# Kernel optimization log

Hardware: AMD Instinct MI355X
Metric: run time of the kernel (lower is better)

## Reference

```python
import jax, jax.numpy as jnp
import numpy as np

EPS = 1e-12  # F.normalize default eps


def setup_inputs() -> dict:
    key = jax.random.key(0)
    x = jax.random.normal(key, (10000, 512), dtype=jnp.float32)
    return {"x": x, "k": 9}


def reference(x, k):
    # F.normalize(x, p=2, dim=0): L2-normalize each feature column over points
    col_norm = jnp.sqrt(jnp.sum(x * x, axis=0, keepdims=True))  # [1, D]
    xn = x / jnp.maximum(col_norm, EPS)                          # [N, D]

    # pairwise squared euclidean distance: ||xi||^2 - 2 xi.xj + ||xj||^2
    sq = jnp.sum(xn * xn, axis=-1, keepdims=True)                # [N, 1]
    dist = sq - 2.0 * (xn @ xn.T) + sq.T                          # [N, N]

    # k nearest neighbors = top-k of negative distance
    _, nn_idx = jax.lax.top_k(-dist, k)                           # [N, k] int32

    n = x.shape[0]
    center_idx = jnp.broadcast_to(jnp.arange(n, dtype=nn_idx.dtype)[:, None], (n, k))
    edge_idx = jnp.stack((nn_idx, center_idx), axis=0)            # [2, N, k]
    return edge_idx
```

## Files before the change

### kernel.cpp

```cpp
#include <hip/hip_runtime.h>
#include <math.h>

#define DD 512
#define NBLKA 400

#define PM 128
#define PN 128
#define KB 32
#define CSPLIT 6
#define NC 12
#define PBUF 32
#define PBSTRIDE 36
#define NCTOT (CSPLIT*NC)
#define KOUTMAX 16
#define RS_MARGIN 2e-4f

typedef __attribute__((ext_vector_type(8))) short bf16x8;
typedef __attribute__((ext_vector_type(4))) float f32x4;

static __device__ __forceinline__ unsigned short f2bf(float f) {
    unsigned u = __float_as_uint(f);
    u += 0x7fff + ((u >> 16) & 1);
    return (unsigned short)(u >> 16);
}

__global__ void colsum_partial(const float* __restrict__ x, double* __restrict__ partial,
                               int N, int rows_per_block) {
    int b = blockIdx.x;
    int t = threadIdx.x;
    int r0 = b * rows_per_block;
    int r1 = min(r0 + rows_per_block, N);
    double s0 = 0.0, s1 = 0.0;
    for (int r = r0; r < r1; ++r) {
        float v0 = x[(size_t)r * DD + t];
        float v1 = x[(size_t)r * DD + t + 256];
        s0 += (double)v0 * (double)v0;
        s1 += (double)v1 * (double)v1;
    }
    partial[(size_t)b * DD + t]       = s0;
    partial[(size_t)b * DD + t + 256] = s1;
}

__global__ void colnorm_finish(const double* __restrict__ partial, double* __restrict__ rn,
                               double* __restrict__ w, int nblk) {
    int c = threadIdx.x;
    double s = 0.0;
    for (int b = 0; b < nblk; ++b) s += partial[(size_t)b * DD + c];
    double n = fmax(sqrt(s), 1e-12);
    double r = 1.0 / n;
    rn[c]  = r;
    w[c]   = r * r;
}

__global__ __launch_bounds__(256) void row_sq(const float* __restrict__ x,
                       const double* __restrict__ rn,
                       double* __restrict__ sq, float* __restrict__ sqf,
                       unsigned short* __restrict__ xnbf, int N) {
    int lane = threadIdx.x & 63;
    int wid  = threadIdx.x >> 6;
    int i = blockIdx.x * 4 + wid;
    if (i >= N) return;

    const float4* xr = (const float4*)(x + (size_t)i * DD);
    float4 v0 = xr[lane];
    float4 v1 = xr[64 + lane];
    const double2* rp = (const double2*)rn;
    double2 r0a = rp[lane * 2],       r0b = rp[lane * 2 + 1];
    double2 r1a = rp[128 + lane * 2], r1b = rp[128 + lane * 2 + 1];

    double a0 = (double)v0.x * r0a.x, a1 = (double)v0.y * r0a.y;
    double a2 = (double)v0.z * r0b.x, a3 = (double)v0.w * r0b.y;
    double b0 = (double)v1.x * r1a.x, b1 = (double)v1.y * r1a.y;
    double b2 = (double)v1.z * r1b.x, b3 = (double)v1.w * r1b.y;

    ushort4 s0 = { f2bf((float)a0), f2bf((float)a1), f2bf((float)a2), f2bf((float)a3) };
    ushort4 s1 = { f2bf((float)b0), f2bf((float)b1), f2bf((float)b2), f2bf((float)b3) };
    *(ushort4*)(xnbf + (size_t)i * DD + lane * 4)       = s0;
    *(ushort4*)(xnbf + (size_t)i * DD + 256 + lane * 4) = s1;

    double loc = a0*a0 + a1*a1 + a2*a2 + a3*a3 + b0*b0 + b1*b1 + b2*b2 + b3*b3;
#pragma unroll
    for (int off = 32; off > 0; off >>= 1)
        loc += __shfl_xor(loc, off, 64);
    if (lane == 0) { sq[i] = loc; sqf[i] = (float)loc; }
}

__global__ __launch_bounds__(256, 2) void gemm_prefilter(
    const unsigned short* __restrict__ xnbf,
    const float* __restrict__ sqf, int* __restrict__ cand, float* __restrict__ cands,
    int N, int ntileM, int ntileN)
{
    __shared__ __align__(16) unsigned char lds_raw[65536];
    __shared__ float sqi_s[PM];
    __shared__ float sqj_s[PN];
    __shared__ float thr_s[PM];
    __shared__ int   cnt_s[PM];
    __shared__ int   flag_s;

    float (*Bsc)[PBSTRIDE] = (float (*)[PBSTRIDE]) lds_raw;
    int   (*Bid)[PBSTRIDE] = (int   (*)[PBSTRIDE]) (lds_raw + 32768);

    const int bid   = blockIdx.x;
    const int q     = bid & 7;
    const int s     = bid >> 3;
    const int ridx  = s / CSPLIT;
    const int split = s - ridx * CSPLIT;
    const int rowb  = q + 8 * ridx;
    if (rowb >= ntileM) return;
    const int row0  = rowb * PM;

    const int t      = threadIdx.x;
    const int lane15 = t & 15;
    const int quad   = (t >> 4) & 3;
    const int wave   = t >> 6;
    const int wr     = (wave >> 1) * 64;
    const int wc     = (wave & 1) * 64;
    const int sl     = quad ^ (lane15 & 3);

    if (t == 0) flag_s = 0;
    if (t < PM) {
        int i = row0 + t;
        sqi_s[t] = (i < N) ? sqf[i] : 0.f;
        thr_s[t] = __builtin_inff();
        cnt_s[t] = 0;
    }

    float ls[NC];
    int   li[NC];
#pragma unroll
    for (int m = 0; m < NC; ++m) { ls[m] = __builtin_inff(); li[m] = 0x7fffffff; }

    f32x4 acc[4][4];

    for (int tile = split; tile < ntileN; tile += CSPLIT) {
        int col0 = tile * PN;

        if (t < PN) {
            int j = col0 + t;
            sqj_s[t] = (j < N) ? sqf[j] : __builtin_inff();
        }
        __syncthreads();

#pragma unroll
        for (int mt = 0; mt < 4; ++mt)
#pragma unroll
            for (int nt = 0; nt < 4; ++nt)
                acc[mt][nt] = (f32x4){0.f, 0.f, 0.f, 0.f};

        auto STAGE = [&](int kc, int buf) {
#pragma unroll
            for (int l = 0; l < 4; ++l) {
                int e      = t + l * 256;
                int region = e >> 9;
                int re     = e & 511;
                int row    = re >> 2;
                int c      = (re & 3) ^ (row & 3);
                int basei  = region ? col0 : row0;
                size_t g = (size_t)(basei + row) * DD + kc + c * 8;
                __builtin_amdgcn_global_load_lds(
                    (const unsigned int*)(xnbf + g),
                    (unsigned int*)(lds_raw + (size_t)buf * 16384 + (size_t)e * 16), 16, 0, 0);
            }
        };

        STAGE(0, 0); STAGE(KB, 1); STAGE(2 * KB, 2);
#pragma unroll 1
        for (int cc = 0; cc < 16; ++cc) {
            if (cc <= 13)      asm volatile("s_waitcnt vmcnt(8)" ::: "memory");
            else if (cc == 14) asm volatile("s_waitcnt vmcnt(4)" ::: "memory");
            else               asm volatile("s_waitcnt vmcnt(0)" ::: "memory");
            __builtin_amdgcn_s_barrier();
            __builtin_amdgcn_sched_barrier(0);
            if (cc + 3 < 16)
                STAGE((cc + 3) * KB, (cc + 3) & 3);
            __builtin_amdgcn_sched_barrier(0);

            const unsigned char* rb = lds_raw + (size_t)(cc & 3) * 16384;
            bf16x8 af[4], bfg[4];
#pragma unroll
            for (int mt = 0; mt < 4; ++mt)
                af[mt] = *(const bf16x8*)(rb + (size_t)(wr + mt * 16 + lane15) * 64 + sl * 16);
#pragma unroll
            for (int nt = 0; nt < 4; ++nt)
                bfg[nt] = *(const bf16x8*)(rb + 8192 + (size_t)(wc + nt * 16 + lane15) * 64 + sl * 16);
#pragma unroll
            for (int mt = 0; mt < 4; ++mt)
#pragma unroll
                for (int nt = 0; nt < 4; ++nt)
                    acc[mt][nt] = __builtin_amdgcn_mfma_f32_16x16x32_bf16(
                        af[mt], bfg[nt], acc[mt][nt], 0, 0, 0);
            __builtin_amdgcn_sched_barrier(0);
        }

#pragma unroll
        for (int mt = 0; mt < 4; ++mt)
#pragma unroll
            for (int nt = 0; nt < 4; ++nt)
#pragma unroll
                for (int reg = 0; reg < 4; ++reg) {
                    int rl = wr + mt * 16 + quad * 4 + reg;
                    int cl = wc + nt * 16 + lane15;
                    float g = acc[mt][nt][reg];
                    acc[mt][nt][reg] = (sqi_s[rl] - 2.f * g) + sqj_s[cl];
                }
        __syncthreads();

        bool tile_edge = (col0 + PN > N);
        unsigned long long done = 0ull;
        for (;;) {
#pragma unroll
            for (int mt = 0; mt < 4; ++mt)
#pragma unroll
                for (int reg = 0; reg < 4; ++reg) {
                    const unsigned long long gb =
                        (0x1111ull << reg) << (mt * 16);
                    int rl = wr + mt * 16 + quad * 4 + reg;
                    float th = thr_s[rl];
                    float gmin = fminf(fminf(acc[mt][0][reg], acc[mt][1][reg]),
                                       fminf(acc[mt][2][reg], acc[mt][3][reg]));
                    if (!tile_edge && gmin > th) { done |= gb; continue; }
                    if ((done & gb) == gb) continue;
#pragma unroll
                    for (int nt = 0; nt < 4; ++nt) {
                        const unsigned long long bit = 1ull << (mt * 16 + nt * 4 + reg);
                        if (!(done & bit)) {
                            float sv = acc[mt][nt][reg];
                            int   j  = col0 + wc + nt * 16 + lane15;
                            if (j < N && sv <= th) {
                                int pos = atomicAdd(&cnt_s[rl], 1);
                                if (pos < PBUF) {
                                    Bsc[rl][pos] = sv;
                                    Bid[rl][pos] = j;
                                    done |= bit;
                                }
                            } else {
                                done |= bit;
                            }
                        }
                    }
                }
            if (done != ~0ull) flag_s = 1;
            __syncthreads();
            if (t < PM) {
                int c = cnt_s[t];
                if (c > PBUF) c = PBUF;
                cnt_s[t] = 0;
                for (int m0 = 0; m0 < c; m0 += 4) {
                    float4 s4 = *(const float4*)&Bsc[t][m0];
                    int4   j4 = *(const int4*)&Bid[t][m0];
#pragma unroll
                    for (int e = 0; e < 4; ++e) {
                        if (m0 + e >= c) break;
                        float sv = (e == 0) ? s4.x : (e == 1) ? s4.y : (e == 2) ? s4.z : s4.w;
                        int   j  = (e == 0) ? j4.x : (e == 1) ? j4.y : (e == 2) ? j4.z : j4.w;
                        if (sv < ls[NC - 1] || (sv == ls[NC - 1] && j < li[NC - 1])) {
                            float cs = sv; int cj = j;
#pragma unroll
                            for (int p = 0; p < NC; ++p) {
                                bool lt = (cs < ls[p]) || (cs == ls[p] && cj < li[p]);
                                float ts = ls[p]; int tj = li[p];
                                if (lt) { ls[p] = cs; li[p] = cj; cs = ts; cj = tj; }
                            }
                        }
                    }
                }
                thr_s[t] = ls[NC - 1];
            }
            __syncthreads();
            int go = flag_s;
            __syncthreads();
            if (t == 0) flag_s = 0;
            __syncthreads();
            if (!go) break;
        }
    }
    if (t < PM) {
        int i = row0 + t;
        if (i < N) {
#pragma unroll
            for (int m = 0; m < NC; ++m) {
                cand [(size_t)i * NCTOT + split * NC + m] = li[m];
                cands[(size_t)i * NCTOT + split * NC + m] = ls[m];
            }
        }
    }
}

__global__ __launch_bounds__(256) void rescore_topk(
    const float* __restrict__ x, const double* __restrict__ w,
    const double* __restrict__ sq, const int* __restrict__ cand,
    const float* __restrict__ cands, int* __restrict__ out, int N, int k)
{
    __shared__ float Ssc[4][NCTOT];
    int lane = threadIdx.x & 63;
    int wid  = threadIdx.x >> 6;
    int i = blockIdx.x * 4 + wid;
    if (i >= N) return;

    size_t base = (size_t)i * NCTOT;
    Ssc[wid][lane] = cands[base + lane];
    if (lane < NCTOT - 64) Ssc[wid][64 + lane] = cands[base + 64 + lane];

    float p0 = Ssc[wid][lane];
    float p1 = Ssc[wid][64 + (lane & 7)];
    int c0 = 0, c1 = 0;
    for (int m = 0; m < NCTOT; ++m) {
        float s = Ssc[wid][m];
        c0 += (s <= p0); c1 += (s <= p1);
    }
    float best = __builtin_inff();
    if (c0 >= k) best = p0;
    if (c1 >= k && p1 < best) best = p1;
#pragma unroll
    for (int off = 32; off > 0; off >>= 1)
        best = fminf(best, __shfl_xor(best, off, 64));
    float cut = best + RS_MARGIN;

    double aw[8];
#pragma unroll
    for (int c = 0; c < 8; ++c) {
        int d = lane + 64 * c;
        aw[c] = (double)x[(size_t)i * DD + d] * w[d];
    }
    double sqi = sq[i];

    double bs[KOUTMAX];
    int    bj[KOUTMAX];
    for (int r = 0; r < k; ++r) { bs[r] = __builtin_inf(); bj[r] = 0x7fffffff; }

    int pend = -1;
    for (int m = 0; m <= NCTOT; ++m) {
        int j1cand = -1;
        if (m < NCTOT) {
            if (Ssc[wid][m] > cut) continue;
            j1cand = cand[base + m];
            if (pend < 0) { pend = j1cand; continue; }
        } else if (pend < 0) {
            break;
        }
        int j0 = pend, j1 = j1cand;
        pend = -1;
        const float* q0 = &x[(size_t)j0 * DD + lane];
        const float* q1 = (j1 >= 0) ? &x[(size_t)j1 * DD + lane] : q0;
        float v0[8], v1[8];
#pragma unroll
        for (int c = 0; c < 8; ++c) v0[c] = q0[64 * c];
#pragma unroll
        for (int c = 0; c < 8; ++c) v1[c] = q1[64 * c];
        double d0 = 0.0, d1 = 0.0;
#pragma unroll
        for (int c = 0; c < 8; ++c) d0 = fma(aw[c], (double)v0[c], d0);
#pragma unroll
        for (int c = 0; c < 8; ++c) d1 = fma(aw[c], (double)v1[c], d1);
#pragma unroll
        for (int off = 32; off > 0; off >>= 1) {
            d0 += __shfl_xor(d0, off, 64);
            d1 += __shfl_xor(d1, off, 64);
        }
        double s0 = (sqi - 2.0 * d0) + sq[j0];
        double s1 = (j1 >= 0) ? (sqi - 2.0 * d1) + sq[j1] : __builtin_inf();
#pragma unroll 1
        for (int pick = 0; pick < 2; ++pick) {
            double sv = pick ? s1 : s0;
            int    j  = pick ? j1 : j0;
            if (j < 0) continue;
            if (sv < bs[k - 1] || (sv == bs[k - 1] && j < bj[k - 1])) {
                int pos = k - 1;
                while (pos > 0) {
                    double ps = bs[pos - 1]; int pj = bj[pos - 1];
                    if (!(sv < ps || (sv == ps && j < pj))) break;
                    bs[pos] = ps; bj[pos] = pj;
                    --pos;
                }
                bs[pos] = sv; bj[pos] = j;
            }
        }
    }
    if (lane == 0) {
        for (int r = 0; r < k; ++r) {
            out[(size_t)i * k + r]                 = bj[r];
            out[(size_t)N * k + (size_t)i * k + r] = i;
        }
    }
}

extern "C" void kernel_launch(void* const* d_in, const int* in_sizes, int n_in,
                              void* d_out, int out_size, void* d_ws, size_t ws_size,
                              hipStream_t stream) {
    const float* x = (const float*)d_in[0];
    int N = in_sizes[0] / DD;
    int k = out_size / (2 * N);
    if (k > KOUTMAX) k = KOUTMAX;

    char* ws = (char*)d_ws;
    double*         partial = (double*)ws;
    double*         rn      = (double*)(ws + 1638400);
    double*         w       = (double*)(ws + 1642496);
    double*         sq      = (double*)(ws + 1646592);
    float*          sqf     = (float*) (ws + 1726592);
    unsigned short* xnbf    = (unsigned short*)(ws + 1766592);
    int*            cand    = (int*)   (ws + 12006592);
    float*          cands   = (float*) (ws + 14886592);

    int rpb = (N + NBLKA - 1) / NBLKA;
    hipLaunchKernelGGL(colsum_partial, dim3(NBLKA), dim3(256), 0, stream, x, partial, N, rpb);
    hipLaunchKernelGGL(colnorm_finish, dim3(1), dim3(512), 0, stream, partial, rn, w, NBLKA);
    hipLaunchKernelGGL(row_sq, dim3((N + 3) / 4), dim3(256), 0, stream, x, rn, sq, sqf, xnbf, N);

    int ntileM = (N + PM - 1) / PM;
    int ntileN = (N + PN - 1) / PN;
    int rows_per_xcd = (ntileM + 7) / 8;
    int nblk = 8 * rows_per_xcd * CSPLIT;
    hipLaunchKernelGGL(gemm_prefilter, dim3(nblk), dim3(256), 0, stream,
                       xnbf, sqf, cand, cands, N, ntileM, ntileN);

    hipLaunchKernelGGL(rescore_topk, dim3((N + 3) / 4), dim3(256), 0, stream,
                       x, w, sq, cand, cands, (int*)d_out, N, k);
}
```

Before: 800.0 us.

## Widen GEMM column tile to 256 and switch to double-buffered staging

```diff
diff --git a/kernel.cpp b/kernel.cpp
--- a/kernel.cpp
+++ b/kernel.cpp
@@ -5,7 +5,7 @@
 #define NBLKA 400
 
 #define PM 128
-#define PN 128
+#define PN 256
 #define KB 32
 #define CSPLIT 6
 #define NC 12
@@ -90,7 +90,7 @@
     const float* __restrict__ sqf, int* __restrict__ cand, float* __restrict__ cands,
     int N, int ntileM, int ntileN)
 {
-    __shared__ __align__(16) unsigned char lds_raw[65536];
+    __shared__ __align__(16) unsigned char lds_raw[49152];
     __shared__ float sqi_s[PM];
     __shared__ float sqj_s[PN];
     __shared__ float thr_s[PM];
@@ -98,7 +98,7 @@
     __shared__ int   flag_s;
 
     float (*Bsc)[PBSTRIDE] = (float (*)[PBSTRIDE]) lds_raw;
-    int   (*Bid)[PBSTRIDE] = (int   (*)[PBSTRIDE]) (lds_raw + 32768);
+    int   (*Bid)[PBSTRIDE] = (int   (*)[PBSTRIDE]) (lds_raw + 24576);
 
     const int bid   = blockIdx.x;
     const int q     = bid & 7;
@@ -114,7 +114,7 @@
     const int quad   = (t >> 4) & 3;
     const int wave   = t >> 6;
     const int wr     = (wave >> 1) * 64;
-    const int wc     = (wave & 1) * 64;
+    const int wc     = (wave & 1) * 128;
     const int sl     = quad ^ (lane15 & 3);
 
     if (t == 0) flag_s = 0;
@@ -130,12 +130,12 @@
 #pragma unroll
     for (int m = 0; m < NC; ++m) { ls[m] = __builtin_inff(); li[m] = 0x7fffffff; }
 
-    f32x4 acc[4][4];
+    f32x4 acc[4][8];
 
     for (int tile = split; tile < ntileN; tile += CSPLIT) {
         int col0 = tile * PN;
 
-        if (t < PN) {
+        {
             int j = col0 + t;
             sqj_s[t] = (j < N) ? sqf[j] : __builtin_inff();
         }
@@ -144,58 +144,69 @@
 #pragma unroll
         for (int mt = 0; mt < 4; ++mt)
 #pragma unroll
-            for (int nt = 0; nt < 4; ++nt)
+            for (int nt = 0; nt < 8; ++nt)
                 acc[mt][nt] = (f32x4){0.f, 0.f, 0.f, 0.f};
 
         auto STAGE = [&](int kc, int buf) {
-#pragma unroll
-            for (int l = 0; l < 4; ++l) {
-                int e      = t + l * 256;
-                int region = e >> 9;
-                int re     = e & 511;
-                int row    = re >> 2;
-                int c      = (re & 3) ^ (row & 3);
-                int basei  = region ? col0 : row0;
-                size_t g = (size_t)(basei + row) * DD + kc + c * 8;
+            unsigned char* base = lds_raw + (size_t)buf * 24576;
+#pragma unroll
+            for (int l = 0; l < 2; ++l) {
+                int e   = t + l * 256;
+                int row = e >> 2;
+                int c   = (e & 3) ^ (row & 3);
+                size_t g = (size_t)(row0 + row) * DD + kc + c * 8;
                 __builtin_amdgcn_global_load_lds(
                     (const unsigned int*)(xnbf + g),
-                    (unsigned int*)(lds_raw + (size_t)buf * 16384 + (size_t)e * 16), 16, 0, 0);
+                    (unsigned int*)(base + (size_t)e * 16), 16, 0, 0);
+            }
+#pragma unroll
+            for (int l = 0; l < 4; ++l) {
+                int e   = t + l * 256;
+                int row = e >> 2;
+                int c   = (e & 3) ^ (row & 3);
+                size_t g = (size_t)(col0 + row) * DD + kc + c * 8;
+                __builtin_amdgcn_global_load_lds(
+                    (const unsigned int*)(xnbf + g),
+                    (unsigned int*)(base + 8192 + (size_t)e * 16), 16, 0, 0);
             }
         };
 
-        STAGE(0, 0); STAGE(KB, 1); STAGE(2 * KB, 2);
+        STAGE(0, 0);
 #pragma unroll 1
         for (int cc = 0; cc < 16; ++cc) {
-            if (cc <= 13)      asm volatile("s_waitcnt vmcnt(8)" ::: "memory");
-            else if (cc == 14) asm volatile("s_waitcnt vmcnt(4)" ::: "memory");
-            else               asm volatile("s_waitcnt vmcnt(0)" ::: "memory");
+            if (cc < 15) {
+                STAGE((cc + 1) * KB, (cc + 1) & 1);
+                __builtin_amdgcn_sched_barrier(0);
+                asm volatile("s_waitcnt vmcnt(6)" ::: "memory");
+            } else {
+                __builtin_amdgcn_sched_barrier(0);
+                asm volatile("s_waitcnt vmcnt(0)" ::: "memory");
+            }
             __builtin_amdgcn_s_barrier();
             __builtin_amdgcn_sched_barrier(0);
-            if (cc + 3 < 16)
-                STAGE((cc + 3) * KB, (cc + 3) & 3);
-            __builtin_amdgcn_sched_barrier(0);
-
-            const unsigned char* rb = lds_raw + (size_t)(cc & 3) * 16384;
-            bf16x8 af[4], bfg[4];
+
+            const unsigned char* rb = lds_raw + (size_t)(cc & 1) * 24576;
+            bf16x8 af[4], bfg[8];
 #pragma unroll
             for (int mt = 0; mt < 4; ++mt)
                 af[mt] = *(const bf16x8*)(rb + (size_t)(wr + mt * 16 + lane15) * 64 + sl * 16);
 #pragma unroll
-            for (int nt = 0; nt < 4; ++nt)
+            for (int nt = 0; nt < 8; ++nt)
                 bfg[nt] = *(const bf16x8*)(rb + 8192 + (size_t)(wc + nt * 16 + lane15) * 64 + sl * 16);
 #pragma unroll
             for (int mt = 0; mt < 4; ++mt)
 #pragma unroll
-                for (int nt = 0; nt < 4; ++nt)
+                for (int nt = 0; nt < 8; ++nt)
                     acc[mt][nt] = __builtin_amdgcn_mfma_f32_16x16x32_bf16(
                         af[mt], bfg[nt], acc[mt][nt], 0, 0, 0);
             __builtin_amdgcn_sched_barrier(0);
+            __builtin_amdgcn_s_barrier();
         }
 
 #pragma unroll
         for (int mt = 0; mt < 4; ++mt)
 #pragma unroll
-            for (int nt = 0; nt < 4; ++nt)
+            for (int nt = 0; nt < 8; ++nt)
 #pragma unroll
                 for (int reg = 0; reg < 4; ++reg) {
                     int rl = wr + mt * 16 + quad * 4 + reg;
@@ -206,40 +217,50 @@
         __syncthreads();
 
         bool tile_edge = (col0 + PN > N);
-        unsigned long long done = 0ull;
+        unsigned long long done0 = 0ull, done1 = 0ull;
         for (;;) {
 #pragma unroll
-            for (int mt = 0; mt < 4; ++mt)
-#pragma unroll
-                for (int reg = 0; reg < 4; ++reg) {
-                    const unsigned long long gb =
-                        (0x1111ull << reg) << (mt * 16);
-                    int rl = wr + mt * 16 + quad * 4 + reg;
-                    float th = thr_s[rl];
-                    float gmin = fminf(fminf(acc[mt][0][reg], acc[mt][1][reg]),
-                                       fminf(acc[mt][2][reg], acc[mt][3][reg]));
-                    if (!tile_edge && gmin > th) { done |= gb; continue; }
-                    if ((done & gb) == gb) continue;
-#pragma unroll
-                    for (int nt = 0; nt < 4; ++nt) {
-                        const unsigned long long bit = 1ull << (mt * 16 + nt * 4 + reg);
-                        if (!(done & bit)) {
-                            float sv = acc[mt][nt][reg];
-                            int   j  = col0 + wc + nt * 16 + lane15;
-                            if (j < N && sv <= th) {
-                                int pos = atomicAdd(&cnt_s[rl], 1);
-                                if (pos < PBUF) {
-                                    Bsc[rl][pos] = sv;
-                                    Bid[rl][pos] = j;
-                                    done |= bit;
+            for (int hn = 0; hn < 2; ++hn) {
+#pragma unroll
+                for (int mt = 0; mt < 4; ++mt)
+#pragma unroll
+                    for (int reg = 0; reg < 4; ++reg) {
+                        const unsigned long long gb =
+                            (0x1111ull << reg) << (mt * 16);
+                        unsigned long long dn = hn ? done1 : done0;
+                        int rl = wr + mt * 16 + quad * 4 + reg;
+                        float th = thr_s[rl];
+                        float gmin = fminf(
+                            fminf(acc[mt][hn * 4 + 0][reg], acc[mt][hn * 4 + 1][reg]),
+                            fminf(acc[mt][hn * 4 + 2][reg], acc[mt][hn * 4 + 3][reg]));
+                        if (!tile_edge && gmin > th) {
+                            if (hn) done1 |= gb; else done0 |= gb;
+                            continue;
+                        }
+                        if ((dn & gb) == gb) continue;
+#pragma unroll
+                        for (int u = 0; u < 4; ++u) {
+                            const unsigned long long bit = 1ull << (mt * 16 + u * 4 + reg);
+                            if (!(dn & bit)) {
+                                float sv = acc[mt][hn * 4 + u][reg];
+                                int   j  = col0 + wc + (hn * 4 + u) * 16 + lane15;
+                                bool ok = false;
+                                if (j < N && sv <= th) {
+                                    int pos = atomicAdd(&cnt_s[rl], 1);
+                                    if (pos < PBUF) {
+                                        Bsc[rl][pos] = sv;
+                                        Bid[rl][pos] = j;
+                                        ok = true;
+                                    }
+                                } else {
+                                    ok = true;
                                 }
-                            } else {
-                                done |= bit;
+                                if (ok) { if (hn) done1 |= bit; else done0 |= bit; }
                             }
                         }
                     }
-                }
-            if (done != ~0ull) flag_s = 1;
+            }
+            if (done0 != ~0ull || done1 != ~0ull) flag_s = 1;
             __syncthreads();
             if (t < PM) {
                 int c = cnt_s[t];
```

New measurement: 706.3 us. 11.7% less time.
